# Performance work log

Hardware: AMD Instinct MI355X
Metric: run time of the kernel (lower is better)

The kernel has to match this reference:

```python
import jax, jax.numpy as jnp
import numpy as np

N = 16_777_216  # total nodes
B = 16_384      # graphs per batch


def setup_inputs() -> dict:
    key = jax.random.key(0)
    ks = jax.random.split(key, 9)
    x = jax.random.normal(ks[0], (N, 1), dtype=jnp.float32)
    batch = jnp.sort(jax.random.randint(ks[1], (N,), 0, B)).astype(jnp.int64)
    node_type = jax.random.randint(ks[2], (N,), 0, 3).astype(jnp.int64)
    # MLP params (torch Linear default-ish init scale)
    W1 = jax.random.normal(ks[3], (4, 32), dtype=jnp.float32) * 0.5
    b1 = jax.random.normal(ks[4], (32,), dtype=jnp.float32) * 0.1
    W2 = jax.random.normal(ks[5], (32, 16), dtype=jnp.float32) * 0.18
    b2 = jax.random.normal(ks[6], (16,), dtype=jnp.float32) * 0.1
    W3 = jax.random.normal(ks[7], (16, 1), dtype=jnp.float32) * 0.25
    b3 = jax.random.normal(ks[8], (1,), dtype=jnp.float32) * 0.1
    return {"x": x, "batch": batch, "node_type": node_type, "num_graphs": B,
            "W1": W1, "b1": b1, "W2": W2, "b2": b2, "W3": W3, "b3": b3}


def reference(x, batch, node_type, num_graphs, W1, b1, W2, b2, W3, b3):
    # Per-graph node-type histogram: one fused segment pass over (N, 4)
    # columns = [count(nt==0), count(nt==1), count(nt==2), total_nodes]
    onehot = jax.nn.one_hot(node_type, 3, dtype=jnp.float32)           # (N, 3)
    per_node = jnp.concatenate([onehot, jnp.ones((onehot.shape[0], 1), jnp.float32)], axis=1)  # (N, 4)
    feats = jax.ops.segment_sum(per_node, batch, num_segments=num_graphs)  # (B, 4)
    feats = feats - jnp.array([54.5, 0.0, 0.0, 56.5], dtype=jnp.float32)
    h = jax.nn.relu(feats @ W1 + b1)
    h = jax.nn.relu(h @ W2 + b2)
    return h @ W3 + b3  # (B, 1)
```

## Files before the change

kernel.cpp:

```cpp
#include <hip/hip_runtime.h>


__global__ __launch_bounds__(256) void bounds_kernel(
    const int* __restrict__ batch, int* __restrict__ S, int n, int nb)
{
    const int g = blockIdx.x * blockDim.x + threadIdx.x;
    if (g > nb) return;
    int lo = 0, hi = n;
    while (lo < hi) {
        int mid = (lo + hi) >> 1;
        if (batch[mid] < g) lo = mid + 1;
        else                hi = mid;
    }
    S[g] = lo;
}

__global__ __launch_bounds__(256) void seg_mlp_kernel(
    const int* __restrict__ ntype, const int* __restrict__ S,
    const float* __restrict__ W1, const float* __restrict__ b1,
    const float* __restrict__ W2, const float* __restrict__ b2,
    const float* __restrict__ W3, const float* __restrict__ b3,
    float* __restrict__ out, int B)
{
    const int t    = blockIdx.x * blockDim.x + threadIdx.x;
    const int g    = t >> 6;
    const int lane = t & 63;
    if (g >= B) return;

    const int s   = S[g];
    const int e   = S[g + 1];
    const int len = e - s;

    int c0 = 0, c1 = 0;

    int sa = (s + 3) & ~3; if (sa > e) sa = e;
    int ea = e & ~3;       if (ea < sa) ea = sa;

    {
        int i = s + lane;
        if (i < sa) { int v = ntype[i]; c0 += (v == 0); c1 += (v == 1); }
    }
    {
        const int4* nt4 = (const int4*)ntype;
        for (int q = (sa >> 2) + lane; q < (ea >> 2); q += 64) {
            int4 v = nt4[q];
            c0 += (v.x == 0) + (v.y == 0) + (v.z == 0) + (v.w == 0);
            c1 += (v.x == 1) + (v.y == 1) + (v.z == 1) + (v.w == 1);
        }
    }
    {
        int i = ea + lane;
        if (i < e) { int v = ntype[i]; c0 += (v == 0); c1 += (v == 1); }
    }

    unsigned long long p = (unsigned)c0 | ((unsigned long long)(unsigned)c1 << 32);
    #pragma unroll
    for (int off = 32; off; off >>= 1) p += __shfl_xor(p, off);
    const int c0t = (int)(p & 0xFFFFFFFFull);
    const int c1t = (int)(p >> 32);

    const float f0 = (float)c0t - 54.5f;
    const float f1 = (float)c1t;
    const float f2 = (float)(len - c0t - c1t);
    const float f3 = (float)len - 56.5f;

    const int j = lane & 31;
    float h1 = b1[j];
    h1 = fmaf(f0, W1[      j], h1);
    h1 = fmaf(f1, W1[ 32 + j], h1);
    h1 = fmaf(f2, W1[ 64 + j], h1);
    h1 = fmaf(f3, W1[ 96 + j], h1);
    h1 = fmaxf(0.0f, h1);

    const int m = lane & 15;
    float s2 = b2[m];
    #pragma unroll
    for (int jj = 0; jj < 32; ++jj) {
        float hj = __shfl(h1, jj);
        s2 = fmaf(hj, W2[jj * 16 + m], s2);
    }
    const float h2 = fmaxf(0.0f, s2);

    float p3 = h2 * W3[m];
    p3 += __shfl_xor(p3, 8);
    p3 += __shfl_xor(p3, 4);
    p3 += __shfl_xor(p3, 2);
    p3 += __shfl_xor(p3, 1);

    if (lane == 0) out[g] = p3 + b3[0];
}

extern "C" void kernel_launch(void* const* d_in, const int* in_sizes, int n_in,
                              void* d_out, int out_size, void* d_ws, size_t ws_size,
                              hipStream_t stream) {
    const int*   batch = (const int*)d_in[1];
    const int*   ntype = (const int*)d_in[2];
    const float* W1    = (const float*)d_in[4];
    const float* b1    = (const float*)d_in[5];
    const float* W2    = (const float*)d_in[6];
    const float* b2    = (const float*)d_in[7];
    const float* W3    = (const float*)d_in[8];
    const float* b3    = (const float*)d_in[9];
    float*       out   = (float*)d_out;

    const int n = in_sizes[1];
    const int B = out_size;

    int* S = (int*)d_ws;

    bounds_kernel<<<(B + 1 + 255) / 256, 256, 0, stream>>>(batch, S, n, B);

    const int total = B * 64;
    seg_mlp_kernel<<<(total + 255) / 256, 256, 0, stream>>>(
        ntype, S, W1, b1, W2, b2, W3, b3, out, B);
}
```

Before: 29.71 us.

## Fuse segment-bounds search into main kernel using wave-wide 64-ary search

Drops the separate bounds kernel and its workspace array. Each wavefront now finds its own segment start and end with a cooperative 64-way ballot search over the sorted batch array, so a 16M-element array is covered in about four rounds instead of a 24-step serial binary search. This removes one kernel launch and the dependency through global memory. In exchange, every wave performs two searches, so the total number of batch loads grows.

```diff
diff --git a/kernel.cpp b/kernel.cpp
--- a/kernel.cpp
+++ b/kernel.cpp
@@ -1,34 +1,38 @@
 #include <hip/hip_runtime.h>
 
 
-__global__ __launch_bounds__(256) void bounds_kernel(
-    const int* __restrict__ batch, int* __restrict__ S, int n, int nb)
+__device__ __forceinline__ int wave_lower_bound(
+    const int* __restrict__ batch, int n, int g, int lane)
 {
-    const int g = blockIdx.x * blockDim.x + threadIdx.x;
-    if (g > nb) return;
-    int lo = 0, hi = n;
-    while (lo < hi) {
-        int mid = (lo + hi) >> 1;
-        if (batch[mid] < g) lo = mid + 1;
-        else                hi = mid;
+    int lo = 0, sz = n;
+    while (sz > 64) {
+        const int step = sz >> 6;
+        const int idx  = lo + (lane + 1) * step;
+        const bool pred = (idx < n) && (batch[idx] < g);
+        const unsigned long long m = __ballot(pred);
+        const int c = __popcll(m);
+        lo += c * step;
+        sz = (c < 64) ? step : (sz - (c << 6) );
     }
-    S[g] = lo;
+    const int idx = lo + lane;
+    const bool pred = (lane < sz) && (idx < n) && (batch[idx] < g);
+    return lo + __popcll(__ballot(pred));
 }
 
-__global__ __launch_bounds__(256) void seg_mlp_kernel(
-    const int* __restrict__ ntype, const int* __restrict__ S,
+__global__ __launch_bounds__(256) void fused_kernel(
+    const int* __restrict__ batch, const int* __restrict__ ntype,
     const float* __restrict__ W1, const float* __restrict__ b1,
     const float* __restrict__ W2, const float* __restrict__ b2,
     const float* __restrict__ W3, const float* __restrict__ b3,
-    float* __restrict__ out, int B)
+    float* __restrict__ out, int n, int B)
 {
     const int t    = blockIdx.x * blockDim.x + threadIdx.x;
     const int g    = t >> 6;
     const int lane = t & 63;
     if (g >= B) return;
 
-    const int s   = S[g];
-    const int e   = S[g + 1];
+    const int s = wave_lower_bound(batch, n, g, lane);
+    const int e = wave_lower_bound(batch, n, g + 1, lane);
     const int len = e - s;
 
     int c0 = 0, c1 = 0;
@@ -37,20 +41,20 @@
     int ea = e & ~3;       if (ea < sa) ea = sa;
 
     {
-        int i = s + lane;
-        if (i < sa) { int v = ntype[i]; c0 += (v == 0); c1 += (v == 1); }
+        const int i = s + lane;
+        if (i < sa) { const int v = ntype[i]; c0 += (v == 0); c1 += (v == 1); }
     }
     {
         const int4* nt4 = (const int4*)ntype;
         for (int q = (sa >> 2) + lane; q < (ea >> 2); q += 64) {
-            int4 v = nt4[q];
+            const int4 v = nt4[q];
             c0 += (v.x == 0) + (v.y == 0) + (v.z == 0) + (v.w == 0);
             c1 += (v.x == 1) + (v.y == 1) + (v.z == 1) + (v.w == 1);
         }
     }
     {
-        int i = ea + lane;
-        if (i < e) { int v = ntype[i]; c0 += (v == 0); c1 += (v == 1); }
+        const int i = ea + lane;
+        if (i < e) { const int v = ntype[i]; c0 += (v == 0); c1 += (v == 1); }
     }
 
     unsigned long long p = (unsigned)c0 | ((unsigned long long)(unsigned)c1 << 32);
@@ -76,7 +80,7 @@
     float s2 = b2[m];
     #pragma unroll
     for (int jj = 0; jj < 32; ++jj) {
-        float hj = __shfl(h1, jj);
+        const float hj = __shfl(h1, jj);
         s2 = fmaf(hj, W2[jj * 16 + m], s2);
     }
     const float h2 = fmaxf(0.0f, s2);
@@ -106,11 +110,8 @@
     const int n = in_sizes[1];
     const int B = out_size;
 
-    int* S = (int*)d_ws;
-
-    bounds_kernel<<<(B + 1 + 255) / 256, 256, 0, stream>>>(batch, S, n, B);
-
-    const int total = B * 64;
-    seg_mlp_kernel<<<(total + 255) / 256, 256, 0, stream>>>(
-        ntype, S, W1, b1, W2, b2, W3, b3, out, B);
+    const long long total = (long long)B * 64;
+    const int blocks = (int)((total + 255) / 256);
+    fused_kernel<<<blocks, 256, 0, stream>>>(
+        batch, ntype, W1, b1, W2, b2, W3, b3, out, n, B);
 }
```

After: 39.12 us. 1.32x slower.

## Narrow bounds search around expected offset and stage MLP weights in LDS

Applied to the files above, without the earlier changes.

The bounds kernel now starts its binary search from a window centred on the expected segment start (g * n/B) and widens it geometrically until the window brackets the boundary. This cuts the number of dependent global loads per thread compared with a full-range search. The MLP kernel stages W1, transposed W2 and the biases in shared memory and computes layer 2 as a float4 dot product from shared memory instead of 32 shuffles with scattered global weight loads. The cost is a block-wide barrier plus an extra __syncthreads in every block, and the windowed search relies on segment sizes being roughly uniform.

```diff
diff --git a/kernel.cpp b/kernel.cpp
--- a/kernel.cpp
+++ b/kernel.cpp
@@ -2,13 +2,24 @@
 
 
 __global__ __launch_bounds__(256) void bounds_kernel(
-    const int* __restrict__ batch, int* __restrict__ S, int n, int nb)
+    const int* __restrict__ batch, int* __restrict__ S, int n, int B)
 {
     const int g = blockIdx.x * blockDim.x + threadIdx.x;
-    if (g > nb) return;
-    int lo = 0, hi = n;
+    if (g > B) return;
+    const long long c = (long long)g * (n / B);
+    int lo, hi;
+    int W = 16384;
+    for (;;) {
+        long long l = c - W, h = c + W;
+        lo = (l < 0) ? 0 : (int)l;
+        hi = (h > n) ? n : (int)h;
+        const bool okL = (lo == 0) || (batch[lo - 1] < g);
+        const bool okR = (hi == n) || (batch[hi] >= g);
+        if (okL && okR) break;
+        W <<= 2;
+    }
     while (lo < hi) {
-        int mid = (lo + hi) >> 1;
+        const int mid = (lo + hi) >> 1;
         if (batch[mid] < g) lo = mid + 1;
         else                hi = mid;
     }
@@ -22,35 +33,51 @@
     const float* __restrict__ W3, const float* __restrict__ b3,
     float* __restrict__ out, int B)
 {
-    const int t    = blockIdx.x * blockDim.x + threadIdx.x;
-    const int g    = t >> 6;
-    const int lane = t & 63;
-    if (g >= B) return;
+    __shared__ __attribute__((aligned(16))) float sW1[128];
+    __shared__ __attribute__((aligned(16))) float sW2T[16 * 36];
+    __shared__ __attribute__((aligned(16))) float sh1[4][32];
+    __shared__ float sb1[32], sb2[16], sW3[16], sb3v[1];
 
-    const int s   = S[g];
-    const int e   = S[g + 1];
+    const int tid = threadIdx.x;
+    if (tid < 128) sW1[tid] = W1[tid];
+    for (int i = tid; i < 512; i += 256) {
+        const int j = i >> 4, m = i & 15;
+        sW2T[m * 36 + j] = W2[i];
+    }
+    if      (tid < 32)  sb1[tid]       = b1[tid];
+    else if (tid < 48)  sb2[tid - 32]  = b2[tid - 32];
+    else if (tid < 64)  sW3[tid - 48]  = W3[tid - 48];
+    else if (tid == 64) sb3v[0]        = b3[0];
+    __syncthreads();
+
+    const int w    = tid >> 6;
+    const int lane = tid & 63;
+    const int g    = blockIdx.x * 4 + w;
+    const bool valid = (g < B);
+
+    const int s = valid ? S[g]     : 0;
+    const int e = valid ? S[g + 1] : 0;
     const int len = e - s;
 
     int c0 = 0, c1 = 0;
-
     int sa = (s + 3) & ~3; if (sa > e) sa = e;
     int ea = e & ~3;       if (ea < sa) ea = sa;
 
     {
-        int i = s + lane;
-        if (i < sa) { int v = ntype[i]; c0 += (v == 0); c1 += (v == 1); }
+        const int i = s + lane;
+        if (i < sa) { const int v = ntype[i]; c0 += (v == 0); c1 += (v == 1); }
     }
     {
         const int4* nt4 = (const int4*)ntype;
         for (int q = (sa >> 2) + lane; q < (ea >> 2); q += 64) {
-            int4 v = nt4[q];
+            const int4 v = nt4[q];
             c0 += (v.x == 0) + (v.y == 0) + (v.z == 0) + (v.w == 0);
             c1 += (v.x == 1) + (v.y == 1) + (v.z == 1) + (v.w == 1);
         }
     }
     {
-        int i = ea + lane;
-        if (i < e) { int v = ntype[i]; c0 += (v == 0); c1 += (v == 1); }
+        const int i = ea + lane;
+        if (i < e) { const int v = ntype[i]; c0 += (v == 0); c1 += (v == 1); }
     }
 
     unsigned long long p = (unsigned)c0 | ((unsigned long long)(unsigned)c1 << 32);
@@ -65,29 +92,37 @@
     const float f3 = (float)len - 56.5f;
 
     const int j = lane & 31;
-    float h1 = b1[j];
-    h1 = fmaf(f0, W1[      j], h1);
-    h1 = fmaf(f1, W1[ 32 + j], h1);
-    h1 = fmaf(f2, W1[ 64 + j], h1);
-    h1 = fmaf(f3, W1[ 96 + j], h1);
+    float h1 = sb1[j];
+    h1 = fmaf(f0, sW1[      j], h1);
+    h1 = fmaf(f1, sW1[ 32 + j], h1);
+    h1 = fmaf(f2, sW1[ 64 + j], h1);
+    h1 = fmaf(f3, sW1[ 96 + j], h1);
     h1 = fmaxf(0.0f, h1);
+    if (lane < 32) sh1[w][j] = h1;
+    __syncthreads();
 
     const int m = lane & 15;
-    float s2 = b2[m];
+    float s2 = sb2[m];
+    const float4* h4  = (const float4*)&sh1[w][0];
+    const float4* wt4 = (const float4*)&sW2T[m * 36];
     #pragma unroll
-    for (int jj = 0; jj < 32; ++jj) {
-        float hj = __shfl(h1, jj);
-        s2 = fmaf(hj, W2[jj * 16 + m], s2);
+    for (int k = 0; k < 8; ++k) {
+        const float4 a = h4[k];
+        const float4 b = wt4[k];
+        s2 = fmaf(a.x, b.x, s2);
+        s2 = fmaf(a.y, b.y, s2);
+        s2 = fmaf(a.z, b.z, s2);
+        s2 = fmaf(a.w, b.w, s2);
     }
     const float h2 = fmaxf(0.0f, s2);
 
-    float p3 = h2 * W3[m];
+    float p3 = h2 * sW3[m];
+    p3 += __shfl_xor(p3, 1);
+    p3 += __shfl_xor(p3, 2);
+    p3 += __shfl_xor(p3, 4);
     p3 += __shfl_xor(p3, 8);
-    p3 += __shfl_xor(p3, 4);
-    p3 += __shfl_xor(p3, 2);
-    p3 += __shfl_xor(p3, 1);
 
-    if (lane == 0) out[g] = p3 + b3[0];
+    if (valid && lane == 0) out[g] = p3 + sb3v[0];
 }
 
 extern "C" void kernel_launch(void* const* d_in, const int* in_sizes, int n_in,
@@ -110,7 +145,6 @@
 
     bounds_kernel<<<(B + 1 + 255) / 256, 256, 0, stream>>>(batch, S, n, B);
 
-    const int total = B * 64;
-    seg_mlp_kernel<<<(total + 255) / 256, 256, 0, stream>>>(
+    seg_mlp_kernel<<<(B + 3) / 4, 256, 0, stream>>>(
         ntype, S, W1, b1, W2, b2, W3, b3, out, B);
 }
```

After: 29.14 us. Within noise of the previous version (-1.9%).
